# Performance work log

Hardware: AMD Instinct MI355X
Metric: run time of the kernel (lower is better)

## Reference

```python
import jax, jax.numpy as jnp
import numpy as np

N_NODES = 100000
N_EDGES = 1600000
IN = 128
HID = 128
EPS = 1e-5


def setup_inputs() -> dict:
    key = jax.random.key(0)
    ks = jax.random.split(key, 20)
    def lin(k, fi, fo):
        return jax.random.normal(k, (fi, fo), dtype=jnp.float32) / np.sqrt(fi)
    inp = {
        'x': jax.random.normal(ks[0], (N_NODES, IN), dtype=jnp.float32),
        'src': jax.random.randint(ks[1], (N_EDGES,), 0, N_NODES),
        'dst': jax.random.randint(ks[2], (N_EDGES,), 0, N_NODES),
        # SAGEConv layer 1..3: fc_self, fc_neigh, bias
        'Wself1': lin(ks[3], IN, HID), 'Wneigh1': lin(ks[4], IN, HID), 'b1': jnp.zeros((HID,), jnp.float32),
        'Wself2': lin(ks[5], HID, HID), 'Wneigh2': lin(ks[6], HID, HID), 'b2': jnp.zeros((HID,), jnp.float32),
        'Wself3': lin(ks[7], HID, HID), 'Wneigh3': lin(ks[8], HID, HID), 'b3': jnp.zeros((HID,), jnp.float32),
        # shared BatchNorm1d(hid)
        'gamma': jnp.ones((HID,), jnp.float32), 'beta': jnp.zeros((HID,), jnp.float32),
        # decoder MLP hid->hid->hid->1
        'Wd1': lin(ks[9], HID, HID), 'bd1': jnp.zeros((HID,), jnp.float32),
        'Wd2': lin(ks[10], HID, HID), 'bd2': jnp.zeros((HID,), jnp.float32),
        'Wd3': lin(ks[11], HID, 1), 'bd3': jnp.zeros((1,), jnp.float32),
    }
    return inp


def _sage_conv(h, src, dst, deg, Wself, Wneigh, b, n):
    # mean aggregation over in-neighbors: gather + segment-sum + divide
    neigh_sum = jax.ops.segment_sum(h[src], dst, num_segments=n)  # [N, F]
    neigh_mean = neigh_sum / deg[:, None]
    return h @ Wself + neigh_mean @ Wneigh + b


def _batch_norm(h, gamma, beta):
    mu = jnp.mean(h, axis=0)
    var = jnp.mean(jnp.square(h - mu), axis=0)  # biased var, as torch BN training
    return gamma * (h - mu) * jax.lax.rsqrt(var + EPS) + beta


def reference(x, src, dst, Wself1, Wneigh1, b1, Wself2, Wneigh2, b2,
              Wself3, Wneigh3, b3, gamma, beta, Wd1, bd1, Wd2, bd2, Wd3, bd3):
    n = x.shape[0]
    deg = jax.ops.segment_sum(jnp.ones_like(dst, dtype=x.dtype), dst, num_segments=n)
    deg = jnp.maximum(deg, 1.0)
    h = _sage_conv(x, src, dst, deg, Wself1, Wneigh1, b1, n)
    h = jax.nn.relu(_batch_norm(h, gamma, beta))  # dropout = identity (eval)
    h = _sage_conv(h, src, dst, deg, Wself2, Wneigh2, b2, n)
    h = jax.nn.relu(_batch_norm(h, gamma, beta))
    h = _sage_conv(h, src, dst, deg, Wself3, Wneigh3, b3, n)
    # decoder MLP
    h = jax.nn.relu(h @ Wd1 + bd1)
    h = jax.nn.relu(h @ Wd2 + bd2)
    return h @ Wd3 + bd3  # [N, 1]
```

## Files before the change

### kernel.cpp

```cpp
#include <hip/hip_runtime.h>

typedef unsigned short u16;
typedef unsigned int u32;
using bf16x8 = __attribute__((ext_vector_type(8))) __bf16;
using f32x4  = __attribute__((ext_vector_type(4))) float;

#define CAP 48
#define LDSROW 136

__global__ void SAGE_79328045957727_kernel() {}

__device__ __forceinline__ float bf2f(u16 u) {
  union { u32 i; float f; } v; v.i = ((u32)u) << 16; return v.f;
}
__device__ __forceinline__ u16 f2bf(float f) {
  union { float f; u32 i; } v; v.f = f;
  u32 x = v.i;
  return (u16)((x + 0x7FFFu + ((x >> 16) & 1u)) >> 16);
}


__global__ void zero_kernel(int* p, int n) {
  int i = blockIdx.x * 256 + threadIdx.x;
  if (i < n) p[i] = 0;
}


__global__ __launch_bounds__(256) void build_kernel(
    const int* __restrict__ src, const int* __restrict__ dst,
    int* __restrict__ deg, int* __restrict__ csr, int E, int npart,
    const float* __restrict__ x, u16* __restrict__ xb, long nelem4,
    const float* w0, const float* w1, const float* w2, const float* w3,
    const float* w4, const float* w5, const float* w6, const float* w7,
    u16* __restrict__ wt) {
  int b = blockIdx.x;
  if (b < 1024) {
    int p = b & 7;
    int brank = b >> 3;
    int lo = p * npart, hi = lo + npart;
    for (int i = brank * 256 + threadIdx.x; i < E; i += 128 * 256) {
      int dv = dst[i];
      if (dv >= lo && dv < hi) {
        int pos = atomicAdd(&deg[dv], 1);
        if (pos < CAP) csr[(size_t)dv * CAP + pos] = src[i];
      }
    }
  } else if (b < 1280) {
    long t = (long)(b - 1024) * 256 + threadIdx.x;
    for (long i4 = t; i4 < nelem4; i4 += 256 * 256) {
      float4 v = ((const float4*)x)[i4];
      u32* op = (u32*)(xb + i4 * 4);
      op[0] = ((u32)f2bf(v.y) << 16) | (u32)f2bf(v.x);
      op[1] = ((u32)f2bf(v.w) << 16) | (u32)f2bf(v.z);
    }
  } else {
    int tg = (b - 1280) * 256 + threadIdx.x;
    for (int k = 0; k < 8; ++k) {
      int idx = tg + k * 16384;
      int m = idx >> 14;
      int i = idx & 16383;
      const float* W = m == 0 ? w0 : m == 1 ? w1 : m == 2 ? w2 : m == 3 ? w3
                     : m == 4 ? w4 : m == 5 ? w5 : m == 6 ? w6 : w7;
      int r = i >> 7, c = i & 127;
      wt[(size_t)m * 16384 + (size_t)c * 128 + r] = f2bf(W[i]);
    }
  }
}


__global__ __launch_bounds__(256) void bnrelu_kernel(
    const u16* __restrict__ Z, u16* __restrict__ G,
    const float* __restrict__ stats, const float* __restrict__ gamma,
    const float* __restrict__ beta, long n4, float invN) {
  __shared__ float sSc[128], sSh[128];
  int t = threadIdx.x;
  if (t < 128) {
    float mu = stats[t] * invN;
    float var = stats[128 + t] * invN - mu * mu;
    float is = rsqrtf(var + 1e-5f);
    float sc = gamma[t] * is;
    sSc[t] = sc;
    sSh[t] = beta[t] - mu * sc;
  }
  __syncthreads();
  for (long i4 = (long)blockIdx.x * 256 + t; i4 < n4; i4 += (long)gridDim.x * 256) {
    uint4 q = ((const uint4*)Z)[i4];
    int c0 = ((int)(i4 & 15)) * 8;
    float e0 = fmaxf(sSc[c0+0]*bf2f((u16)(q.x & 0xffffu))+sSh[c0+0], 0.f);
    float e1 = fmaxf(sSc[c0+1]*bf2f((u16)(q.x >> 16))    +sSh[c0+1], 0.f);
    float e2 = fmaxf(sSc[c0+2]*bf2f((u16)(q.y & 0xffffu))+sSh[c0+2], 0.f);
    float e3 = fmaxf(sSc[c0+3]*bf2f((u16)(q.y >> 16))    +sSh[c0+3], 0.f);
    float e4 = fmaxf(sSc[c0+4]*bf2f((u16)(q.z & 0xffffu))+sSh[c0+4], 0.f);
    float e5 = fmaxf(sSc[c0+5]*bf2f((u16)(q.z >> 16))    +sSh[c0+5], 0.f);
    float e6 = fmaxf(sSc[c0+6]*bf2f((u16)(q.w & 0xffffu))+sSh[c0+6], 0.f);
    float e7 = fmaxf(sSc[c0+7]*bf2f((u16)(q.w >> 16))    +sSh[c0+7], 0.f);
    uint4 o;
    o.x = ((u32)f2bf(e1) << 16) | (u32)f2bf(e0);
    o.y = ((u32)f2bf(e3) << 16) | (u32)f2bf(e2);
    o.z = ((u32)f2bf(e5) << 16) | (u32)f2bf(e4);
    o.w = ((u32)f2bf(e7) << 16) | (u32)f2bf(e6);
    ((uint4*)G)[i4] = o;
  }
}


__device__ __forceinline__ void gather_tile(
    const u16* __restrict__ G, const int* __restrict__ csr,
    const int* __restrict__ deg, u16* sT, size_t row0, int N, int tid) {
  int lf = tid & 15;
  int slot = tid >> 4;
  int fo = lf * 8;
#define ACC8(q) do { \
    a0 += bf2f((u16)((q).x & 0xffffu)); a1 += bf2f((u16)((q).x >> 16)); \
    a2 += bf2f((u16)((q).y & 0xffffu)); a3 += bf2f((u16)((q).y >> 16)); \
    a4 += bf2f((u16)((q).z & 0xffffu)); a5 += bf2f((u16)((q).z >> 16)); \
    a6 += bf2f((u16)((q).w & 0xffffu)); a7 += bf2f((u16)((q).w >> 16)); \
  } while (0)
  for (int it = 0; it < 8; ++it) {
    int r = it * 16 + slot;
    size_t node = row0 + r;
    int d = (node < (size_t)N) ? deg[node] : 0;
    int dm = d < CAP ? d : CAP;
    const int* nl = csr + (node < (size_t)N ? node : 0) * CAP;
    float a0=0.f,a1=0.f,a2=0.f,a3=0.f,a4=0.f,a5=0.f,a6=0.f,a7=0.f;
    int e = 0;
    for (; e + 4 <= dm; e += 4) {
      int i0 = nl[e], i1 = nl[e + 1], i2 = nl[e + 2], i3 = nl[e + 3];
      uint4 q0 = *(const uint4*)(G + (size_t)i0 * 128 + fo);
      uint4 q1 = *(const uint4*)(G + (size_t)i1 * 128 + fo);
      uint4 q2 = *(const uint4*)(G + (size_t)i2 * 128 + fo);
      uint4 q3 = *(const uint4*)(G + (size_t)i3 * 128 + fo);
      ACC8(q0); ACC8(q1); ACC8(q2); ACC8(q3);
    }
    for (; e < dm; ++e) {
      uint4 q = *(const uint4*)(G + (size_t)nl[e] * 128 + fo);
      ACC8(q);
    }
    float inv = 1.f / (float)(d > 0 ? d : 1);
    u32 o0 = ((u32)f2bf(a1 * inv) << 16) | (u32)f2bf(a0 * inv);
    u32 o1 = ((u32)f2bf(a3 * inv) << 16) | (u32)f2bf(a2 * inv);
    u32 o2 = ((u32)f2bf(a5 * inv) << 16) | (u32)f2bf(a4 * inv);
    u32 o3 = ((u32)f2bf(a7 * inv) << 16) | (u32)f2bf(a6 * inv);
    u32* lp = (u32*)(sT + (size_t)r * LDSROW) + lf * 4;
    lp[0] = o0; lp[1] = o1; lp[2] = o2; lp[3] = o3;
  }
#undef ACC8
}

__device__ __forceinline__ void stage_tile(
    const u16* __restrict__ A, u16* sT, size_t row0, int N, int tid) {
  for (int j = 0; j < 8; ++j) {
    int idx = j * 1024 + tid * 4;
    int r = idx >> 6;
    int c = idx & 63;
    size_t grow = row0 + r;
    if (grow >= (size_t)N) grow = (size_t)(N - 1);
    const u32* gp = (const u32*)(A + grow * 128) + c;
    u32 v0 = gp[0], v1 = gp[1], v2 = gp[2], v3 = gp[3];
    u32* lp = (u32*)(sT + (size_t)r * LDSROW + c * 2);
    lp[0] = v0; lp[1] = v1; lp[2] = v2; lp[3] = v3;
  }
}

__device__ __forceinline__ void mfma_tile(
    const u16* sT, const u16* __restrict__ Wt, f32x4 acc[8][2],
    int wave, int l15, int quad) {
  bf16x8 wf[2][4];
  for (int ct = 0; ct < 2; ++ct) {
    int col = wave * 32 + ct * 16 + l15;
    for (int kk = 0; kk < 4; ++kk)
      wf[ct][kk] = *(const bf16x8*)(Wt + (size_t)col * 128 + kk * 32 + quad * 8);
  }
  for (int kk = 0; kk < 4; ++kk) {
    int kbase = kk * 32 + quad * 8;
    for (int rt = 0; rt < 8; ++rt) {
      bf16x8 af = *(const bf16x8*)(sT + (size_t)(rt * 16 + l15) * LDSROW + kbase);
      acc[rt][0] = __builtin_amdgcn_mfma_f32_16x16x32_bf16(af, wf[0][kk], acc[rt][0], 0, 0, 0);
      acc[rt][1] = __builtin_amdgcn_mfma_f32_16x16x32_bf16(af, wf[1][kk], acc[rt][1], 0, 0, 0);
    }
  }
}


__global__ __launch_bounds__(256) void gemm_fused(
    const u16* __restrict__ G, const int* __restrict__ csr,
    const int* __restrict__ deg, const u16* __restrict__ Wst,
    const u16* __restrict__ Wnt, const float* __restrict__ bias,
    u16* __restrict__ C, float* __restrict__ statsOut, int N) {
  __shared__ u16 sT[128 * LDSROW];
  int tid = threadIdx.x;
  int wave = tid >> 6;
  int lane = tid & 63;
  int l15 = lane & 15;
  int quad = lane >> 4;
  size_t row0 = (size_t)blockIdx.x * 128;

  f32x4 acc[8][2];
  for (int rt = 0; rt < 8; ++rt)
    for (int ct = 0; ct < 2; ++ct)
      for (int i = 0; i < 4; ++i) acc[rt][ct][i] = 0.f;

  gather_tile(G, csr, deg, sT, row0, N, tid);
  __syncthreads();
  mfma_tile(sT, Wnt, acc, wave, l15, quad);
  __syncthreads();

  stage_tile(G, sT, row0, N, tid);
  __syncthreads();
  mfma_tile(sT, Wst, acc, wave, l15, quad);

  for (int ct = 0; ct < 2; ++ct) {
    int col = wave * 32 + ct * 16 + l15;
    float bv = bias[col];
    float ssum = 0.f, ssq = 0.f;
    for (int rt = 0; rt < 8; ++rt) {
      for (int i = 0; i < 4; ++i) {
        size_t row = row0 + rt * 16 + quad * 4 + i;
        if (row < (size_t)N) {
          float v = acc[rt][ct][i] + bv;
          C[row * 128 + col] = f2bf(v);
          ssum += v; ssq += v * v;
        }
      }
    }
    for (int o = 16; o < 64; o <<= 1) {
      ssum += __shfl_xor(ssum, o);
      ssq  += __shfl_xor(ssq, o);
    }
    if (quad == 0) {
      atomicAdd(&statsOut[col], ssum);
      atomicAdd(&statsOut[128 + col], ssq);
    }
  }
}


__global__ __launch_bounds__(256) void megagemm(
    const u16* __restrict__ G, const int* __restrict__ csr,
    const int* __restrict__ deg,
    const u16* __restrict__ wtS3, const u16* __restrict__ wtN3,
    const float* __restrict__ b3,
    const u16* __restrict__ wtD1, const float* __restrict__ bd1,
    const u16* __restrict__ wtD2, const float* __restrict__ bd2,
    const float* __restrict__ wd3, const float* __restrict__ bd3,
    float* __restrict__ outF, int N) {
  __shared__ u16 sT[128 * LDSROW];
  __shared__ float sOut[128];

  int tid = threadIdx.x;
  int wave = tid >> 6;
  int lane = tid & 63;
  int l15 = lane & 15;
  int quad = lane >> 4;
  size_t row0 = (size_t)blockIdx.x * 128;

  if (tid < 128) sOut[tid] = 0.f;

  f32x4 acc[8][2];
  for (int rt = 0; rt < 8; ++rt)
    for (int ct = 0; ct < 2; ++ct)
      for (int i = 0; i < 4; ++i) acc[rt][ct][i] = 0.f;

  gather_tile(G, csr, deg, sT, row0, N, tid);
  __syncthreads();
  mfma_tile(sT, wtN3, acc, wave, l15, quad);
  __syncthreads();
  stage_tile(G, sT, row0, N, tid);
  __syncthreads();
  mfma_tile(sT, wtS3, acc, wave, l15, quad);

  for (int g = 0; g < 2; ++g) {
    const u16* Wt = g ? wtD2 : wtD1;
    const float* bs = g ? bd1 : b3;
    int do_relu = g;

    __syncthreads();
    for (int ct = 0; ct < 2; ++ct) {
      int col = wave * 32 + ct * 16 + l15;
      float bv = bs[col];
      for (int rt = 0; rt < 8; ++rt) {
        for (int i = 0; i < 4; ++i) {
          int row = rt * 16 + quad * 4 + i;
          float v = acc[rt][ct][i] + bv;
          if (do_relu) v = fmaxf(v, 0.f);
          sT[(size_t)row * LDSROW + col] = f2bf(v);
        }
      }
    }
    __syncthreads();

    for (int rt = 0; rt < 8; ++rt)
      for (int ct = 0; ct < 2; ++ct)
        for (int i = 0; i < 4; ++i) acc[rt][ct][i] = 0.f;
    mfma_tile(sT, Wt, acc, wave, l15, quad);
  }

  {
    int col0 = wave * 32 + l15;
    float bv0 = bd2[col0], bv1 = bd2[col0 + 16];
    float w30 = wd3[col0], w31 = wd3[col0 + 16];
    for (int rt = 0; rt < 8; ++rt) {
      for (int i = 0; i < 4; ++i) {
        size_t row = row0 + rt * 16 + quad * 4 + i;
        float v0 = fmaxf(acc[rt][0][i] + bv0, 0.f);
        float v1 = fmaxf(acc[rt][1][i] + bv1, 0.f);
        float pv = v0 * w30 + v1 * w31;
        pv += __shfl_xor(pv, 1);
        pv += __shfl_xor(pv, 2);
        pv += __shfl_xor(pv, 4);
        pv += __shfl_xor(pv, 8);
        if (l15 == 0 && row < (size_t)N)
          atomicAdd(&sOut[rt * 16 + quad * 4 + i], pv);
      }
    }
    __syncthreads();
    if (tid < 128) {
      size_t row = row0 + tid;
      if (row < (size_t)N) outF[row] = sOut[tid] + bd3[0];
    }
  }
}


extern "C" void kernel_launch(void* const* d_in, const int* in_sizes, int n_in,
                              void* d_out, int out_size, void* d_ws, size_t ws_size,
                              hipStream_t stream) {
  const float* x      = (const float*)d_in[0];
  const int*   src    = (const int*)d_in[1];
  const int*   dst    = (const int*)d_in[2];
  const float* Wself1 = (const float*)d_in[3];
  const float* Wneigh1= (const float*)d_in[4];
  const float* b1     = (const float*)d_in[5];
  const float* Wself2 = (const float*)d_in[6];
  const float* Wneigh2= (const float*)d_in[7];
  const float* b2     = (const float*)d_in[8];
  const float* Wself3 = (const float*)d_in[9];
  const float* Wneigh3= (const float*)d_in[10];
  const float* b3     = (const float*)d_in[11];
  const float* gamma  = (const float*)d_in[12];
  const float* beta   = (const float*)d_in[13];
  const float* Wd1    = (const float*)d_in[14];
  const float* bd1    = (const float*)d_in[15];
  const float* Wd2    = (const float*)d_in[16];
  const float* bd2    = (const float*)d_in[17];
  const float* Wd3    = (const float*)d_in[18];
  const float* bd3    = (const float*)d_in[19];
  float* out = (float*)d_out;

  int N = in_sizes[0] / 128;
  int E = in_sizes[1];
  int npart = (N + 7) / 8;

  char* ws = (char*)d_ws;
  size_t off = 0;
  int* deg; int* csr; float* stats1; float* stats2;
  u16* xb; u16* ZA; u16* ZB; u16* M; u16* wt;
  deg   = (int*)(ws + off);   off += (size_t)N * 4;
  stats1= (float*)(ws + off); off += 256 * 4;
  stats2= (float*)(ws + off); off += 256 * 4;
  off = (off + 511) & ~(size_t)511;
  csr  = (int*)(ws + off);   off += ((size_t)N * CAP * 4 + 511) & ~(size_t)511;
  wt   = (u16*)(ws + off);   off += ((size_t)8 * 16384 * 2 + 511) & ~(size_t)511;
  xb   = (u16*)(ws + off);   off += ((size_t)N * 128 * 2 + 511) & ~(size_t)511;
  ZA   = (u16*)(ws + off);   off += ((size_t)N * 128 * 2 + 511) & ~(size_t)511;
  ZB   = (u16*)(ws + off);   off += ((size_t)N * 128 * 2 + 511) & ~(size_t)511;
  M    = (u16*)(ws + off);   off += ((size_t)N * 128 * 2 + 511) & ~(size_t)511;

  u16* wtS1 = wt + 0 * 16384; u16* wtN1 = wt + 1 * 16384;
  u16* wtS2 = wt + 2 * 16384; u16* wtN2 = wt + 3 * 16384;
  u16* wtS3 = wt + 4 * 16384; u16* wtN3 = wt + 5 * 16384;
  u16* wtD1 = wt + 6 * 16384; u16* wtD2 = wt + 7 * 16384;

  u16* GA = M;
  u16* GB = ZA;

  zero_kernel<<<(N + 512 + 255) / 256, 256, 0, stream>>>(deg, N + 512);

  long nelem4 = (long)N * 128 / 4;
  build_kernel<<<1344, 256, 0, stream>>>(
      src, dst, deg, csr, E, npart, x, xb, nelem4,
      Wself1, Wneigh1, Wself2, Wneigh2, Wself3, Wneigh3, Wd1, Wd2, wt);

  int strips = (N + 127) / 128;
  float invN = 1.f / (float)N;
  long n4 = (long)N * 16;

  gemm_fused<<<strips, 256, 0, stream>>>(
      xb, csr, deg, wtS1, wtN1, b1, ZA, stats1, N);

  bnrelu_kernel<<<2048, 256, 0, stream>>>(ZA, GA, stats1, gamma, beta, n4, invN);

  gemm_fused<<<strips, 256, 0, stream>>>(
      GA, csr, deg, wtS2, wtN2, b2, ZB, stats2, N);

  bnrelu_kernel<<<2048, 256, 0, stream>>>(ZB, GB, stats2, gamma, beta, n4, invN);

  megagemm<<<strips, 256, 0, stream>>>(
      GB, csr, deg, wtS3, wtN3, b3, wtD1, bd1, wtD2, bd2, Wd3, bd3, out, N);
}
```

Baseline: 649.6 us.

## Split neighbor gather into standalone kernel and double CSR build blocks

Moves mean-aggregation gather out of the fused GEMM kernels into a separate gather_kernel with 16 nodes per block (782 blocks → ~6250 blocks) and 8-way unrolled loads, writing the mean to a global buffer that the GEMMs then stage like dense input. This aims to increase parallelism and latency hiding for the irregular gather instead of having only strips-many blocks do it before MFMA. It adds an extra global write and read of an N×128 bf16 buffer per layer and three more launches. The CSR build also uses twice as many blocks, and bnrelu now writes in place.

```diff
diff --git a/kernel.cpp b/kernel.cpp
--- a/kernel.cpp
+++ b/kernel.cpp
@@ -34,19 +34,19 @@
     const float* w4, const float* w5, const float* w6, const float* w7,
     u16* __restrict__ wt) {
   int b = blockIdx.x;
-  if (b < 1024) {
+  if (b < 2048) {
     int p = b & 7;
     int brank = b >> 3;
     int lo = p * npart, hi = lo + npart;
-    for (int i = brank * 256 + threadIdx.x; i < E; i += 128 * 256) {
+    for (int i = brank * 256 + threadIdx.x; i < E; i += 256 * 256) {
       int dv = dst[i];
       if (dv >= lo && dv < hi) {
         int pos = atomicAdd(&deg[dv], 1);
         if (pos < CAP) csr[(size_t)dv * CAP + pos] = src[i];
       }
     }
-  } else if (b < 1280) {
-    long t = (long)(b - 1024) * 256 + threadIdx.x;
+  } else if (b < 2304) {
+    long t = (long)(b - 2048) * 256 + threadIdx.x;
     for (long i4 = t; i4 < nelem4; i4 += 256 * 256) {
       float4 v = ((const float4*)x)[i4];
       u32* op = (u32*)(xb + i4 * 4);
@@ -54,7 +54,7 @@
       op[1] = ((u32)f2bf(v.w) << 16) | (u32)f2bf(v.z);
     }
   } else {
-    int tg = (b - 1280) * 256 + threadIdx.x;
+    int tg = (b - 2304) * 256 + threadIdx.x;
     for (int k = 0; k < 8; ++k) {
       int idx = tg + k * 16384;
       int m = idx >> 14;
@@ -104,48 +104,64 @@
 }
 
 
-__device__ __forceinline__ void gather_tile(
+__global__ __launch_bounds__(256) void gather_kernel(
     const u16* __restrict__ G, const int* __restrict__ csr,
-    const int* __restrict__ deg, u16* sT, size_t row0, int N, int tid) {
-  int lf = tid & 15;
-  int slot = tid >> 4;
-  int fo = lf * 8;
+    const int* __restrict__ deg, u16* __restrict__ M, int N) {
+  int node = blockIdx.x * 16 + (threadIdx.x >> 4);
+  if (node >= N) return;
+  int lane = threadIdx.x & 15;
+  int fo = lane * 8;
+  const int* nl = csr + (size_t)node * CAP;
+  int d = deg[node];
+  int dm = d < CAP ? d : CAP;
+  float a0=0.f,a1=0.f,a2=0.f,a3=0.f,a4=0.f,a5=0.f,a6=0.f,a7=0.f;
+
 #define ACC8(q) do { \
     a0 += bf2f((u16)((q).x & 0xffffu)); a1 += bf2f((u16)((q).x >> 16)); \
     a2 += bf2f((u16)((q).y & 0xffffu)); a3 += bf2f((u16)((q).y >> 16)); \
     a4 += bf2f((u16)((q).z & 0xffffu)); a5 += bf2f((u16)((q).z >> 16)); \
     a6 += bf2f((u16)((q).w & 0xffffu)); a7 += bf2f((u16)((q).w >> 16)); \
   } while (0)
-  for (int it = 0; it < 8; ++it) {
-    int r = it * 16 + slot;
-    size_t node = row0 + r;
-    int d = (node < (size_t)N) ? deg[node] : 0;
-    int dm = d < CAP ? d : CAP;
-    const int* nl = csr + (node < (size_t)N ? node : 0) * CAP;
-    float a0=0.f,a1=0.f,a2=0.f,a3=0.f,a4=0.f,a5=0.f,a6=0.f,a7=0.f;
-    int e = 0;
-    for (; e + 4 <= dm; e += 4) {
-      int i0 = nl[e], i1 = nl[e + 1], i2 = nl[e + 2], i3 = nl[e + 3];
-      uint4 q0 = *(const uint4*)(G + (size_t)i0 * 128 + fo);
-      uint4 q1 = *(const uint4*)(G + (size_t)i1 * 128 + fo);
-      uint4 q2 = *(const uint4*)(G + (size_t)i2 * 128 + fo);
-      uint4 q3 = *(const uint4*)(G + (size_t)i3 * 128 + fo);
-      ACC8(q0); ACC8(q1); ACC8(q2); ACC8(q3);
-    }
-    for (; e < dm; ++e) {
-      uint4 q = *(const uint4*)(G + (size_t)nl[e] * 128 + fo);
-      ACC8(q);
-    }
-    float inv = 1.f / (float)(d > 0 ? d : 1);
-    u32 o0 = ((u32)f2bf(a1 * inv) << 16) | (u32)f2bf(a0 * inv);
-    u32 o1 = ((u32)f2bf(a3 * inv) << 16) | (u32)f2bf(a2 * inv);
-    u32 o2 = ((u32)f2bf(a5 * inv) << 16) | (u32)f2bf(a4 * inv);
-    u32 o3 = ((u32)f2bf(a7 * inv) << 16) | (u32)f2bf(a6 * inv);
-    u32* lp = (u32*)(sT + (size_t)r * LDSROW) + lf * 4;
-    lp[0] = o0; lp[1] = o1; lp[2] = o2; lp[3] = o3;
+
+  int e = 0;
+  for (; e + 8 <= dm; e += 8) {
+    int ia = nl[e+0], ib = nl[e+1], ic = nl[e+2], id_ = nl[e+3];
+    int ie_ = nl[e+4], if_ = nl[e+5], ig = nl[e+6], ih = nl[e+7];
+    uint4 q0 = *(const uint4*)(G + (size_t)ia  * 128 + fo);
+    uint4 q1 = *(const uint4*)(G + (size_t)ib  * 128 + fo);
+    uint4 q2 = *(const uint4*)(G + (size_t)ic  * 128 + fo);
+    uint4 q3 = *(const uint4*)(G + (size_t)id_ * 128 + fo);
+    uint4 q4 = *(const uint4*)(G + (size_t)ie_ * 128 + fo);
+    uint4 q5 = *(const uint4*)(G + (size_t)if_ * 128 + fo);
+    uint4 q6 = *(const uint4*)(G + (size_t)ig  * 128 + fo);
+    uint4 q7 = *(const uint4*)(G + (size_t)ih  * 128 + fo);
+    ACC8(q0); ACC8(q1); ACC8(q2); ACC8(q3);
+    ACC8(q4); ACC8(q5); ACC8(q6); ACC8(q7);
+  }
+  if (e + 4 <= dm) {
+    int ia = nl[e+0], ib = nl[e+1], ic = nl[e+2], id_ = nl[e+3];
+    uint4 q0 = *(const uint4*)(G + (size_t)ia  * 128 + fo);
+    uint4 q1 = *(const uint4*)(G + (size_t)ib  * 128 + fo);
+    uint4 q2 = *(const uint4*)(G + (size_t)ic  * 128 + fo);
+    uint4 q3 = *(const uint4*)(G + (size_t)id_ * 128 + fo);
+    ACC8(q0); ACC8(q1); ACC8(q2); ACC8(q3);
+    e += 4;
+  }
+  for (; e < dm; ++e) {
+    uint4 q = *(const uint4*)(G + (size_t)nl[e] * 128 + fo);
+    ACC8(q);
   }
 #undef ACC8
-}
+
+  float inv = 1.f / (float)(d > 0 ? d : 1);
+  uint4 o;
+  o.x = ((u32)f2bf(a1 * inv) << 16) | (u32)f2bf(a0 * inv);
+  o.y = ((u32)f2bf(a3 * inv) << 16) | (u32)f2bf(a2 * inv);
+  o.z = ((u32)f2bf(a5 * inv) << 16) | (u32)f2bf(a4 * inv);
+  o.w = ((u32)f2bf(a7 * inv) << 16) | (u32)f2bf(a6 * inv);
+  *(uint4*)(M + (size_t)node * 128 + fo) = o;
+}
+
 
 __device__ __forceinline__ void stage_tile(
     const u16* __restrict__ A, u16* sT, size_t row0, int N, int tid) {
@@ -182,11 +198,11 @@
 }
 
 
-__global__ __launch_bounds__(256) void gemm_fused(
-    const u16* __restrict__ G, const int* __restrict__ csr,
-    const int* __restrict__ deg, const u16* __restrict__ Wst,
-    const u16* __restrict__ Wnt, const float* __restrict__ bias,
-    u16* __restrict__ C, float* __restrict__ statsOut, int N) {
+__global__ __launch_bounds__(256) void gemm2(
+    const u16* __restrict__ A, const u16* __restrict__ B,
+    const u16* __restrict__ W1t, const u16* __restrict__ W2t,
+    const float* __restrict__ bias, u16* __restrict__ C,
+    float* __restrict__ statsOut, int N) {
   __shared__ u16 sT[128 * LDSROW];
   int tid = threadIdx.x;
   int wave = tid >> 6;
@@ -200,14 +216,13 @@
     for (int ct = 0; ct < 2; ++ct)
       for (int i = 0; i < 4; ++i) acc[rt][ct][i] = 0.f;
 
-  gather_tile(G, csr, deg, sT, row0, N, tid);
-  __syncthreads();
-  mfma_tile(sT, Wnt, acc, wave, l15, quad);
-  __syncthreads();
-
-  stage_tile(G, sT, row0, N, tid);
-  __syncthreads();
-  mfma_tile(sT, Wst, acc, wave, l15, quad);
+  stage_tile(A, sT, row0, N, tid);
+  __syncthreads();
+  mfma_tile(sT, W1t, acc, wave, l15, quad);
+  __syncthreads();
+  stage_tile(B, sT, row0, N, tid);
+  __syncthreads();
+  mfma_tile(sT, W2t, acc, wave, l15, quad);
 
   for (int ct = 0; ct < 2; ++ct) {
     int col = wave * 32 + ct * 16 + l15;
@@ -236,8 +251,7 @@
 
 
 __global__ __launch_bounds__(256) void megagemm(
-    const u16* __restrict__ G, const int* __restrict__ csr,
-    const int* __restrict__ deg,
+    const u16* __restrict__ G, const u16* __restrict__ M,
     const u16* __restrict__ wtS3, const u16* __restrict__ wtN3,
     const float* __restrict__ b3,
     const u16* __restrict__ wtD1, const float* __restrict__ bd1,
@@ -261,7 +275,7 @@
     for (int ct = 0; ct < 2; ++ct)
       for (int i = 0; i < 4; ++i) acc[rt][ct][i] = 0.f;
 
-  gather_tile(G, csr, deg, sT, row0, N, tid);
+  stage_tile(M, sT, row0, N, tid);
   __syncthreads();
   mfma_tile(sT, wtN3, acc, wave, l15, quad);
   __syncthreads();
@@ -371,30 +385,29 @@
   u16* wtS3 = wt + 4 * 16384; u16* wtN3 = wt + 5 * 16384;
   u16* wtD1 = wt + 6 * 16384; u16* wtD2 = wt + 7 * 16384;
 
-  u16* GA = M;
-  u16* GB = ZA;
-
   zero_kernel<<<(N + 512 + 255) / 256, 256, 0, stream>>>(deg, N + 512);
 
   long nelem4 = (long)N * 128 / 4;
-  build_kernel<<<1344, 256, 0, stream>>>(
+  build_kernel<<<2368, 256, 0, stream>>>(
       src, dst, deg, csr, E, npart, x, xb, nelem4,
       Wself1, Wneigh1, Wself2, Wneigh2, Wself3, Wneigh3, Wd1, Wd2, wt);
 
   int strips = (N + 127) / 128;
+  int g16    = (N + 15) / 16;
   float invN = 1.f / (float)N;
   long n4 = (long)N * 16;
 
-  gemm_fused<<<strips, 256, 0, stream>>>(
-      xb, csr, deg, wtS1, wtN1, b1, ZA, stats1, N);
-
-  bnrelu_kernel<<<2048, 256, 0, stream>>>(ZA, GA, stats1, gamma, beta, n4, invN);
-
-  gemm_fused<<<strips, 256, 0, stream>>>(
-      GA, csr, deg, wtS2, wtN2, b2, ZB, stats2, N);
-
-  bnrelu_kernel<<<2048, 256, 0, stream>>>(ZB, GB, stats2, gamma, beta, n4, invN);
-
+  gather_kernel<<<g16, 256, 0, stream>>>(xb, csr, deg, M, N);
+  gemm2<<<strips, 256, 0, stream>>>(xb, M, wtS1, wtN1, b1, ZA, stats1, N);
+
+  bnrelu_kernel<<<2048, 256, 0, stream>>>(ZA, ZA, stats1, gamma, beta, n4, invN);
+
+  gather_kernel<<<g16, 256, 0, stream>>>(ZA, csr, deg, M, N);
+  gemm2<<<strips, 256, 0, stream>>>(ZA, M, wtS2, wtN2, b2, ZB, stats2, N);
+
+  bnrelu_kernel<<<2048, 256, 0, stream>>>(ZB, ZB, stats2, gamma, beta, n4, invN);
+
+  gather_kernel<<<g16, 256, 0, stream>>>(ZB, csr, deg, M, N);
   megagemm<<<strips, 256, 0, stream>>>(
-      GB, csr, deg, wtS3, wtN3, b3, wtD1, bd1, wtD2, bd2, Wd3, bd3, out, N);
-}
+      ZB, M, wtS3, wtN3, b3, wtD1, bd1, wtD2, bd2, Wd3, bd3, out, N);
+}
```

After: 564.8 us. -13.0%, faster.
